# Kernel optimization log

Measured on AMD Instinct MI355X. Metric: run time of the kernel, lower is better.

## Reference

```python
import jax, jax.numpy as jnp
import numpy as np

B = 32
H_TEX, W_TEX, C = 512, 512, 3
N = H_TEX * W_TEX * C          # flattened texture length per sample
OH, OW = 128, 64               # bbox_size
M = OH * OW * C                # rows of each per-sample sparse matrix
NNZ = 98304                    # nonzeros per sample (4 per output element)


def setup_inputs() -> dict:
    key = jax.random.key(0)
    k1, k2, k3, k4 = jax.random.split(key, 4)
    x = jax.random.normal(k1, (B, C, H_TEX, W_TEX), dtype=jnp.float32)
    rows = jax.random.randint(k2, (B, NNZ), 0, M, dtype=jnp.int32)
    cols = jax.random.randint(k3, (B, NNZ), 0, N, dtype=jnp.int32)
    vals = jax.random.uniform(k4, (B, NNZ), dtype=jnp.float32)
    mask = jnp.ones((B, C, OH, OW), dtype=jnp.float32)
    return {"x": x, "rows": rows, "cols": cols, "vals": vals, "mask": mask}


def reference(x, rows, cols, vals, mask):
    # x: (B, C, H, W) -> channels-last flat per sample, matching x.permute(0,2,3,1).reshape(B,-1)
    xf = jnp.transpose(x, (0, 2, 3, 1)).reshape(B, -1)          # (B, N)
    # Batched sparse mm: out[b, m] = sum_{k: rows[b,k]==m} vals[b,k] * xf[b, cols[b,k]]
    gathered = vals * jnp.take_along_axis(xf, cols, axis=1)     # (B, NNZ)
    seg_ids = (rows.astype(jnp.int32) + jnp.arange(B, dtype=jnp.int32)[:, None] * M).reshape(-1)
    out_flat = jax.ops.segment_sum(gathered.reshape(-1), seg_ids, num_segments=B * M)
    result = out_flat.reshape(B, OH, OW, C).transpose(0, 3, 1, 2)  # (B, C, 128, 64)
    return result, mask
```

## Files before the change

kernel.cpp:

```cpp
#include <hip/hip_runtime.h>

#define BATCH 32
#define CCH 3
#define HW_TEX (512 * 512)
#define N_TEX (HW_TEX * CCH)
#define OH 128
#define OW 64
#define P_OUT (OH * OW)
#define M_OUT (P_OUT * CCH)
#define NNZ 98304
#define OUT_ELEMS (BATCH * M_OUT)

#define NCH 4
#define RPCH (M_OUT / NCH)
#define NE 8
#define SEGE (NNZ / NE)
#define TB 1024
#define NROUND 4

#define WS_NEED ((size_t)BATCH * NCH * NE * RPCH * 4)

__global__ __launch_bounds__(TB) void scan_pred8_kernel(
    const float* __restrict__ x,
    const int*   __restrict__ rows,
    const int*   __restrict__ cols,
    const float* __restrict__ vals,
    float* __restrict__ partial) {
    __shared__ __align__(16) float acc[RPCH];

    const int blk  = blockIdx.x;
    const int xcd  = blk & 7;
    const int slot = blk >> 3;
    const int c    = slot & (NCH - 1);
    const int e    = slot >> 2;
    const int t    = threadIdx.x;
    const int rbase = c * RPCH;

    for (int rnd = 0; rnd < NROUND; ++rnd) {
        const int s = rnd * 8 + xcd;

        float2* acc2 = reinterpret_cast<float2*>(acc);
#pragma unroll
        for (int j = 0; j < RPCH / 2 / TB; ++j)
            acc2[t + j * TB] = make_float2(0.f, 0.f);
        __syncthreads();

        const size_t off = (size_t)s * NNZ + (size_t)e * SEGE;
        const int4*   r4 = reinterpret_cast<const int4*>(rows + off);
        const int4*   c4 = reinterpret_cast<const int4*>(cols + off);
        const float4* v4 = reinterpret_cast<const float4*>(vals + off);
        const float*  xs = x + (size_t)s * N_TEX;

        int4 r[3], cc[3]; float4 v[3];
#pragma unroll
        for (int j = 0; j < 3; ++j) {
            r[j]  = r4[j * TB + t];
            cc[j] = c4[j * TB + t];
            v[j]  = v4[j * TB + t];
        }

#pragma unroll
        for (int j = 0; j < 3; ++j) {
            int   ri[4] = {r[j].x, r[j].y, r[j].z, r[j].w};
            int   ci[4] = {cc[j].x, cc[j].y, cc[j].z, cc[j].w};
            float vi[4] = {v[j].x, v[j].y, v[j].z, v[j].w};
#pragma unroll
            for (int k = 0; k < 4; ++k) {
                unsigned lr = (unsigned)(ri[k] - rbase);
                if (lr < (unsigned)RPCH) {
                    int gi = (ci[k] % CCH) * HW_TEX + ci[k] / CCH;
                    atomicAdd(&acc[lr], vi[k] * xs[gi]);
                }
            }
        }
        __syncthreads();

        float2* pp = reinterpret_cast<float2*>(
            partial + (((size_t)s * NCH + c) * NE + e) * RPCH);
#pragma unroll
        for (int j = 0; j < RPCH / 2 / TB; ++j)
            pp[t + j * TB] = acc2[t + j * TB];
        __syncthreads();
    }
}

__global__ __launch_bounds__(256) void reduce_chunk_kernel(
    const float* __restrict__ partial,
    const float* __restrict__ mask,
    float* __restrict__ out) {
    int tid = blockIdx.x * 256 + threadIdx.x;
    if (tid >= OUT_ELEMS / 4) return;
    int s    = tid / (M_OUT / 4);
    int rcl4 = (tid % (M_OUT / 4)) * 4;
    int c    = rcl4 / RPCH;
    int lr4  = rcl4 % RPCH;

    const float4* pp = reinterpret_cast<const float4*>(
        partial + (((size_t)s * NCH + c) * NE) * RPCH + lr4);
    float4 sum = make_float4(0.f, 0.f, 0.f, 0.f);
#pragma unroll
    for (int e = 0; e < NE; ++e) {
        float4 p = pp[(size_t)e * (RPCH / 4)];
        sum.x += p.x; sum.y += p.y; sum.z += p.z; sum.w += p.w;
    }
    float* ob = out + (size_t)s * M_OUT;
    ob[(rcl4 + 0) % CCH * P_OUT + (rcl4 + 0) / CCH] = sum.x;
    ob[(rcl4 + 1) % CCH * P_OUT + (rcl4 + 1) / CCH] = sum.y;
    ob[(rcl4 + 2) % CCH * P_OUT + (rcl4 + 2) / CCH] = sum.z;
    ob[(rcl4 + 3) % CCH * P_OUT + (rcl4 + 3) / CCH] = sum.w;
    reinterpret_cast<float4*>(out + OUT_ELEMS)[tid] =
        reinterpret_cast<const float4*>(mask)[tid];
}

#define CHUNKS 8
#define RPC (M_OUT / CHUNKS)
#define BLOCK 1024
__global__ __launch_bounds__(BLOCK) void spmm_chunk_kernel(
    const float* __restrict__ x,
    const int*   __restrict__ rows,
    const int*   __restrict__ cols,
    const float* __restrict__ vals,
    const float* __restrict__ mask,
    float* __restrict__ out) {
    __shared__ float acc[RPC];
    const int blk = blockIdx.x;
    const int s   = blk / CHUNKS;
    const int c   = blk % CHUNKS;
    const int t   = threadIdx.x;
    const int rbase = c * RPC;
#pragma unroll
    for (int j = 0; j < RPC / BLOCK; ++j) acc[t + j * BLOCK] = 0.0f;
    __syncthreads();
    const int*   rs = rows + (size_t)s * NNZ;
    const int*   cs = cols + (size_t)s * NNZ;
    const float* vs = vals + (size_t)s * NNZ;
    const float* xs = x    + (size_t)s * N_TEX;
#pragma unroll 4
    for (int i = t; i < NNZ; i += BLOCK) {
        int r = rs[i];
        unsigned lr = (unsigned)(r - rbase);
        if (lr < (unsigned)RPC) {
            int   col = cs[i];
            float v   = vs[i];
            atomicAdd(&acc[lr], v * xs[(col % CCH) * HW_TEX + col / CCH]);
        }
    }
    __syncthreads();
    const size_t outbase = (size_t)s * M_OUT;
#pragma unroll
    for (int ch = 0; ch < CCH; ++ch)
        out[outbase + (size_t)ch * P_OUT + c * (P_OUT / CHUNKS) + t] = acc[t * CCH + ch];
    {
        float* mout = out + OUT_ELEMS;
        const int base = blk * RPC;
#pragma unroll
        for (int j = 0; j < RPC / BLOCK; ++j)
            mout[base + j * BLOCK + t] = mask[base + j * BLOCK + t];
    }
}

extern "C" void kernel_launch(void* const* d_in, const int* in_sizes, int n_in,
                              void* d_out, int out_size, void* d_ws, size_t ws_size,
                              hipStream_t stream) {
    const float* x    = (const float*)d_in[0];
    const int*   rows = (const int*)  d_in[1];
    const int*   cols = (const int*)  d_in[2];
    const float* vals = (const float*)d_in[3];
    const float* mask = (const float*)d_in[4];
    float* out = (float*)d_out;
    int rgrid = (OUT_ELEMS / 4 + 255) / 256;

    if (ws_size >= WS_NEED) {
        float* partial = (float*)d_ws;
        scan_pred8_kernel<<<256, TB, 0, stream>>>(x, rows, cols, vals, partial);
        reduce_chunk_kernel<<<rgrid, 256, 0, stream>>>(partial, mask, out);
    } else {
        spmm_chunk_kernel<<<BATCH * CHUNKS, BLOCK, 0, stream>>>(x, rows, cols, vals, mask, out);
    }
}
```

Before: 208.8 us.

## Replace chunked LDS accumulation with direct global atomic scatter

Drops the LDS-chunked predicated scan and the partial-sum reduction. A zero-init kernel now clears the output and copies the mask, then each thread scatters its nonzeros straight into the output with global float atomicAdd. This removes the redundant rescans of the index stream across row chunks and the workspace round trip. The cost is global atomic traffic on random addresses and a summation order that is no longer deterministic.

```diff
diff --git a/kernel.cpp b/kernel.cpp
--- a/kernel.cpp
+++ b/kernel.cpp
@@ -11,152 +11,55 @@
 #define NNZ 98304
 #define OUT_ELEMS (BATCH * M_OUT)
 
-#define NCH 4
-#define RPCH (M_OUT / NCH)
-#define NE 8
-#define SEGE (NNZ / NE)
-#define TB 1024
+#define SC_TB 1024
 #define NROUND 4
 
-#define WS_NEED ((size_t)BATCH * NCH * NE * RPCH * 4)
-
-__global__ __launch_bounds__(TB) void scan_pred8_kernel(
+__global__ __launch_bounds__(SC_TB) void scatter_kernel(
     const float* __restrict__ x,
     const int*   __restrict__ rows,
     const int*   __restrict__ cols,
     const float* __restrict__ vals,
-    float* __restrict__ partial) {
-    __shared__ __align__(16) float acc[RPCH];
-
+    float* __restrict__ out) {
     const int blk  = blockIdx.x;
     const int xcd  = blk & 7;
     const int slot = blk >> 3;
-    const int c    = slot & (NCH - 1);
-    const int e    = slot >> 2;
     const int t    = threadIdx.x;
-    const int rbase = c * RPCH;
+    const int base = slot * SC_TB + t;
 
     for (int rnd = 0; rnd < NROUND; ++rnd) {
         const int s = rnd * 8 + xcd;
+        const size_t ib = (size_t)s * NNZ;
+        const float* xs = x + (size_t)s * N_TEX;
+        float* os = out + (size_t)s * M_OUT;
 
-        float2* acc2 = reinterpret_cast<float2*>(acc);
-#pragma unroll
-        for (int j = 0; j < RPCH / 2 / TB; ++j)
-            acc2[t + j * TB] = make_float2(0.f, 0.f);
-        __syncthreads();
+        int   r0 = rows[ib + base];
+        int   r1 = rows[ib + base + 32768];
+        int   r2 = rows[ib + base + 65536];
+        int   c0 = cols[ib + base];
+        int   c1 = cols[ib + base + 32768];
+        int   c2 = cols[ib + base + 65536];
+        float v0 = vals[ib + base];
+        float v1 = vals[ib + base + 32768];
+        float v2 = vals[ib + base + 65536];
 
-        const size_t off = (size_t)s * NNZ + (size_t)e * SEGE;
-        const int4*   r4 = reinterpret_cast<const int4*>(rows + off);
-        const int4*   c4 = reinterpret_cast<const int4*>(cols + off);
-        const float4* v4 = reinterpret_cast<const float4*>(vals + off);
-        const float*  xs = x + (size_t)s * N_TEX;
+        float x0 = xs[(c0 % CCH) * HW_TEX + c0 / CCH];
+        float x1 = xs[(c1 % CCH) * HW_TEX + c1 / CCH];
+        float x2 = xs[(c2 % CCH) * HW_TEX + c2 / CCH];
 
-        int4 r[3], cc[3]; float4 v[3];
-#pragma unroll
-        for (int j = 0; j < 3; ++j) {
-            r[j]  = r4[j * TB + t];
-            cc[j] = c4[j * TB + t];
-            v[j]  = v4[j * TB + t];
-        }
-
-#pragma unroll
-        for (int j = 0; j < 3; ++j) {
-            int   ri[4] = {r[j].x, r[j].y, r[j].z, r[j].w};
-            int   ci[4] = {cc[j].x, cc[j].y, cc[j].z, cc[j].w};
-            float vi[4] = {v[j].x, v[j].y, v[j].z, v[j].w};
-#pragma unroll
-            for (int k = 0; k < 4; ++k) {
-                unsigned lr = (unsigned)(ri[k] - rbase);
-                if (lr < (unsigned)RPCH) {
-                    int gi = (ci[k] % CCH) * HW_TEX + ci[k] / CCH;
-                    atomicAdd(&acc[lr], vi[k] * xs[gi]);
-                }
-            }
-        }
-        __syncthreads();
-
-        float2* pp = reinterpret_cast<float2*>(
-            partial + (((size_t)s * NCH + c) * NE + e) * RPCH);
-#pragma unroll
-        for (int j = 0; j < RPCH / 2 / TB; ++j)
-            pp[t + j * TB] = acc2[t + j * TB];
-        __syncthreads();
+        atomicAdd(&os[(r0 % CCH) * P_OUT + r0 / CCH], v0 * x0);
+        atomicAdd(&os[(r1 % CCH) * P_OUT + r1 / CCH], v1 * x1);
+        atomicAdd(&os[(r2 % CCH) * P_OUT + r2 / CCH], v2 * x2);
     }
 }
 
-__global__ __launch_bounds__(256) void reduce_chunk_kernel(
-    const float* __restrict__ partial,
+__global__ __launch_bounds__(256) void init_out_kernel(
     const float* __restrict__ mask,
     float* __restrict__ out) {
     int tid = blockIdx.x * 256 + threadIdx.x;
     if (tid >= OUT_ELEMS / 4) return;
-    int s    = tid / (M_OUT / 4);
-    int rcl4 = (tid % (M_OUT / 4)) * 4;
-    int c    = rcl4 / RPCH;
-    int lr4  = rcl4 % RPCH;
-
-    const float4* pp = reinterpret_cast<const float4*>(
-        partial + (((size_t)s * NCH + c) * NE) * RPCH + lr4);
-    float4 sum = make_float4(0.f, 0.f, 0.f, 0.f);
-#pragma unroll
-    for (int e = 0; e < NE; ++e) {
-        float4 p = pp[(size_t)e * (RPCH / 4)];
-        sum.x += p.x; sum.y += p.y; sum.z += p.z; sum.w += p.w;
-    }
-    float* ob = out + (size_t)s * M_OUT;
-    ob[(rcl4 + 0) % CCH * P_OUT + (rcl4 + 0) / CCH] = sum.x;
-    ob[(rcl4 + 1) % CCH * P_OUT + (rcl4 + 1) / CCH] = sum.y;
-    ob[(rcl4 + 2) % CCH * P_OUT + (rcl4 + 2) / CCH] = sum.z;
-    ob[(rcl4 + 3) % CCH * P_OUT + (rcl4 + 3) / CCH] = sum.w;
+    reinterpret_cast<float4*>(out)[tid] = make_float4(0.f, 0.f, 0.f, 0.f);
     reinterpret_cast<float4*>(out + OUT_ELEMS)[tid] =
         reinterpret_cast<const float4*>(mask)[tid];
-}
-
-#define CHUNKS 8
-#define RPC (M_OUT / CHUNKS)
-#define BLOCK 1024
-__global__ __launch_bounds__(BLOCK) void spmm_chunk_kernel(
-    const float* __restrict__ x,
-    const int*   __restrict__ rows,
-    const int*   __restrict__ cols,
-    const float* __restrict__ vals,
-    const float* __restrict__ mask,
-    float* __restrict__ out) {
-    __shared__ float acc[RPC];
-    const int blk = blockIdx.x;
-    const int s   = blk / CHUNKS;
-    const int c   = blk % CHUNKS;
-    const int t   = threadIdx.x;
-    const int rbase = c * RPC;
-#pragma unroll
-    for (int j = 0; j < RPC / BLOCK; ++j) acc[t + j * BLOCK] = 0.0f;
-    __syncthreads();
-    const int*   rs = rows + (size_t)s * NNZ;
-    const int*   cs = cols + (size_t)s * NNZ;
-    const float* vs = vals + (size_t)s * NNZ;
-    const float* xs = x    + (size_t)s * N_TEX;
-#pragma unroll 4
-    for (int i = t; i < NNZ; i += BLOCK) {
-        int r = rs[i];
-        unsigned lr = (unsigned)(r - rbase);
-        if (lr < (unsigned)RPC) {
-            int   col = cs[i];
-            float v   = vs[i];
-            atomicAdd(&acc[lr], v * xs[(col % CCH) * HW_TEX + col / CCH]);
-        }
-    }
-    __syncthreads();
-    const size_t outbase = (size_t)s * M_OUT;
-#pragma unroll
-    for (int ch = 0; ch < CCH; ++ch)
-        out[outbase + (size_t)ch * P_OUT + c * (P_OUT / CHUNKS) + t] = acc[t * CCH + ch];
-    {
-        float* mout = out + OUT_ELEMS;
-        const int base = blk * RPC;
-#pragma unroll
-        for (int j = 0; j < RPC / BLOCK; ++j)
-            mout[base + j * BLOCK + t] = mask[base + j * BLOCK + t];
-    }
 }
 
 extern "C" void kernel_launch(void* const* d_in, const int* in_sizes, int n_in,
@@ -168,13 +71,8 @@
     const float* vals = (const float*)d_in[3];
     const float* mask = (const float*)d_in[4];
     float* out = (float*)d_out;
-    int rgrid = (OUT_ELEMS / 4 + 255) / 256;
 
-    if (ws_size >= WS_NEED) {
-        float* partial = (float*)d_ws;
-        scan_pred8_kernel<<<256, TB, 0, stream>>>(x, rows, cols, vals, partial);
-        reduce_chunk_kernel<<<rgrid, 256, 0, stream>>>(partial, mask, out);
-    } else {
-        spmm_chunk_kernel<<<BATCH * CHUNKS, BLOCK, 0, stream>>>(x, rows, cols, vals, mask, out);
-    }
+    int igrid = (OUT_ELEMS / 4 + 255) / 256;
+    init_out_kernel<<<igrid, 256, 0, stream>>>(mask, out);
+    scatter_kernel<<<256, SC_TB, 0, stream>>>(x, rows, cols, vals, out);
 }
```

Result: slower. 304.0 us (+45.6%).

## Stage COO indices and gathered texels into LDS via global_load_lds

Applied to the files above, without the earlier changes.

Index, column and value arrays are now tiled and loaded straight into LDS with the global_load_lds builtin. The predicated texel gathers also go through direct-to-LDS loads, followed by a vmcnt wait and a separate LDS atomic-accumulate pass. The aim is to cut VGPR pressure and put the random gathers in flight together. In exchange it adds a barrier per tile and splits the gather and accumulate phases, which may reduce overlap. The gather destination relies on the per-lane M0/LDS addressing semantics of that builtin.

```diff
diff --git a/kernel.cpp b/kernel.cpp
--- a/kernel.cpp
+++ b/kernel.cpp
@@ -17,8 +17,21 @@
 #define SEGE (NNZ / NE)
 #define TB 1024
 #define NROUND 4
+#define TILE 3072
+#define EPT 3
 
 #define WS_NEED ((size_t)BATCH * NCH * NE * RPCH * 4)
+
+__device__ __forceinline__ void gld_lds16(const void* g, void* l) {
+    __builtin_amdgcn_global_load_lds(
+        (const __attribute__((address_space(1))) void*)g,
+        (__attribute__((address_space(3))) void*)l, 16, 0, 0);
+}
+__device__ __forceinline__ void gld_lds4(const void* g, void* l) {
+    __builtin_amdgcn_global_load_lds(
+        (const __attribute__((address_space(1))) void*)g,
+        (__attribute__((address_space(3))) void*)l, 4, 0, 0);
+}
 
 __global__ __launch_bounds__(TB) void scan_pred8_kernel(
     const float* __restrict__ x,
@@ -27,6 +40,8 @@
     const float* __restrict__ vals,
     float* __restrict__ partial) {
     __shared__ __align__(16) float acc[RPCH];
+    __shared__ __align__(16) int   s_idx[3][TILE];
+    __shared__ __align__(16) float s_gath[TILE];
 
     const int blk  = blockIdx.x;
     const int xcd  = blk & 7;
@@ -34,6 +49,8 @@
     const int c    = slot & (NCH - 1);
     const int e    = slot >> 2;
     const int t    = threadIdx.x;
+    const int lane = t & 63;
+    const int w    = t >> 6;
     const int rbase = c * RPCH;
 
     for (int rnd = 0; rnd < NROUND; ++rnd) {
@@ -46,34 +63,45 @@
         __syncthreads();
 
         const size_t off = (size_t)s * NNZ + (size_t)e * SEGE;
-        const int4*   r4 = reinterpret_cast<const int4*>(rows + off);
-        const int4*   c4 = reinterpret_cast<const int4*>(cols + off);
-        const float4* v4 = reinterpret_cast<const float4*>(vals + off);
-        const float*  xs = x + (size_t)s * N_TEX;
-
-        int4 r[3], cc[3]; float4 v[3];
-#pragma unroll
-        for (int j = 0; j < 3; ++j) {
-            r[j]  = r4[j * TB + t];
-            cc[j] = c4[j * TB + t];
-            v[j]  = v4[j * TB + t];
-        }
-
-#pragma unroll
-        for (int j = 0; j < 3; ++j) {
-            int   ri[4] = {r[j].x, r[j].y, r[j].z, r[j].w};
-            int   ci[4] = {cc[j].x, cc[j].y, cc[j].z, cc[j].w};
-            float vi[4] = {v[j].x, v[j].y, v[j].z, v[j].w};
-#pragma unroll
-            for (int k = 0; k < 4; ++k) {
-                unsigned lr = (unsigned)(ri[k] - rbase);
-                if (lr < (unsigned)RPCH) {
-                    int gi = (ci[k] % CCH) * HW_TEX + ci[k] / CCH;
-                    atomicAdd(&acc[lr], vi[k] * xs[gi]);
+        const float* xs = x + (size_t)s * N_TEX;
+        const int* gsrc[3] = { rows + off, cols + off,
+                               reinterpret_cast<const int*>(vals + off) };
+
+        for (int tt = 0; tt < SEGE / TILE; ++tt) {
+            const int toff = tt * TILE;
+
+            for (int q = w; q < 36; q += 16) {
+                const int arr = q / 12, sub = q % 12;
+                gld_lds16(gsrc[arr] + toff + sub * 256 + lane * 4,
+                          &s_idx[arr][sub * 256]);
+            }
+            __syncthreads();
+
+#pragma unroll
+            for (int k = 0; k < EPT; ++k) {
+                const int n = w * (EPT * 64) + k * 64 + lane;
+                int rI = s_idx[0][n];
+                int cI = s_idx[1][n];
+                unsigned l = (unsigned)(rI - rbase);
+                if (l < (unsigned)RPCH) {
+                    int gi = (cI % CCH) * HW_TEX + cI / CCH;
+                    gld_lds4(xs + gi, &s_gath[w * (EPT * 64) + k * 64]);
                 }
             }
+            asm volatile("s_waitcnt vmcnt(0)" ::: "memory");
+            __builtin_amdgcn_sched_barrier(0);
+
+#pragma unroll
+            for (int k = 0; k < EPT; ++k) {
+                const int n = w * (EPT * 64) + k * 64 + lane;
+                unsigned l = (unsigned)(s_idx[0][n] - rbase);
+                if (l < (unsigned)RPCH) {
+                    float vv = __int_as_float(s_idx[2][n]);
+                    atomicAdd(&acc[l], vv * s_gath[n]);
+                }
+            }
+            __syncthreads();
         }
-        __syncthreads();
 
         float2* pp = reinterpret_cast<float2*>(
             partial + (((size_t)s * NCH + c) * NE + e) * RPCH);
```

Result: slower. 223.0 us (+6.8%).

## Split rows into 2 chunks and nnz into 16 segments, batching gathers before atomics

Applied to the files above, without the earlier changes.

Adds a new scan/reduce path in which each block owns half the output rows (a 48KB LDS accumulator) and a 1/16 slice of the nonzeros, so each entry is scanned by only 2 blocks instead of 4. It also issues all 6 predicated texture gathers before doing the LDS atomics, to raise memory-level parallelism. In exchange the reduce kernel sums 16 partials instead of 8, and the larger LDS footprint may limit occupancy. The new path runs when the workspace is large enough, otherwise the older paths are kept.

```diff
diff --git a/kernel.cpp b/kernel.cpp
--- a/kernel.cpp
+++ b/kernel.cpp
@@ -11,14 +11,121 @@
 #define NNZ 98304
 #define OUT_ELEMS (BATCH * M_OUT)
 
+#define TB 1024
+#define NROUND 4
+
+#define NCH2 2
+#define RPCH2 (M_OUT / NCH2)
+#define NE2 16
+#define SEGE2 (NNZ / NE2)
+#define EPT2 6
+#define WS_NEED2 ((size_t)BATCH * NCH2 * NE2 * RPCH2 * 4)
+
 #define NCH 4
 #define RPCH (M_OUT / NCH)
 #define NE 8
 #define SEGE (NNZ / NE)
-#define TB 1024
-#define NROUND 4
-
+#define EPT 12
 #define WS_NEED ((size_t)BATCH * NCH * NE * RPCH * 4)
+
+__global__ __launch_bounds__(TB) void scan2_kernel(
+    const float* __restrict__ x,
+    const int*   __restrict__ rows,
+    const int*   __restrict__ cols,
+    const float* __restrict__ vals,
+    float* __restrict__ partial) {
+    __shared__ __align__(16) float acc[RPCH2];
+
+    const int blk  = blockIdx.x;
+    const int xcd  = blk & 7;
+    const int slot = blk >> 3;
+    const int c    = slot & (NCH2 - 1);
+    const int e    = slot >> 1;
+    const int t    = threadIdx.x;
+    const int rbase = c * RPCH2;
+
+    for (int rnd = 0; rnd < NROUND; ++rnd) {
+        const int s = rnd * 8 + xcd;
+
+        float2* acc2 = reinterpret_cast<float2*>(acc);
+#pragma unroll
+        for (int j = 0; j < RPCH2 / 2 / TB; ++j)
+            acc2[t + j * TB] = make_float2(0.f, 0.f);
+        __syncthreads();
+
+        const size_t off = (size_t)s * NNZ + (size_t)e * SEGE2;
+        const int2*   r2 = reinterpret_cast<const int2*>(rows + off);
+        const int2*   c2 = reinterpret_cast<const int2*>(cols + off);
+        const float2* v2 = reinterpret_cast<const float2*>(vals + off);
+        const float*  xs = x + (size_t)s * N_TEX;
+
+        int2 rr[3], cc[3]; float2 vv[3];
+#pragma unroll
+        for (int j = 0; j < 3; ++j) {
+            rr[j] = r2[t + j * TB];
+            cc[j] = c2[t + j * TB];
+            vv[j] = v2[t + j * TB];
+        }
+        int ri[EPT2]; int ci[EPT2]; float vi[EPT2];
+#pragma unroll
+        for (int j = 0; j < 3; ++j) {
+            ri[2 * j] = rr[j].x; ri[2 * j + 1] = rr[j].y;
+            ci[2 * j] = cc[j].x; ci[2 * j + 1] = cc[j].y;
+            vi[2 * j] = vv[j].x; vi[2 * j + 1] = vv[j].y;
+        }
+
+        float xv[EPT2];
+#pragma unroll
+        for (int i = 0; i < EPT2; ++i) {
+            unsigned l = (unsigned)(ri[i] - rbase);
+            int gi = (ci[i] % CCH) * HW_TEX + ci[i] / CCH;
+            xv[i] = xs[(l < (unsigned)RPCH2) ? gi : 0];
+        }
+
+#pragma unroll
+        for (int i = 0; i < EPT2; ++i) {
+            unsigned l = (unsigned)(ri[i] - rbase);
+            if (l < (unsigned)RPCH2)
+                atomicAdd(&acc[l], vi[i] * xv[i]);
+        }
+        __syncthreads();
+
+        float2* pp = reinterpret_cast<float2*>(
+            partial + (((size_t)s * NCH2 + c) * NE2 + e) * RPCH2);
+#pragma unroll
+        for (int j = 0; j < RPCH2 / 2 / TB; ++j)
+            pp[t + j * TB] = acc2[t + j * TB];
+        __syncthreads();
+    }
+}
+
+__global__ __launch_bounds__(256) void reduce2_kernel(
+    const float* __restrict__ partial,
+    const float* __restrict__ mask,
+    float* __restrict__ out) {
+    int tid = blockIdx.x * 256 + threadIdx.x;
+    if (tid >= OUT_ELEMS / 4) return;
+    int s    = tid / (M_OUT / 4);
+    int rcl4 = (tid % (M_OUT / 4)) * 4;
+    int c    = rcl4 / RPCH2;
+    int lr4  = rcl4 % RPCH2;
+
+    const float4* pp = reinterpret_cast<const float4*>(
+        partial + (((size_t)s * NCH2 + c) * NE2) * RPCH2 + lr4);
+    float4 sum = make_float4(0.f, 0.f, 0.f, 0.f);
+#pragma unroll
+    for (int e = 0; e < NE2; ++e) {
+        float4 p = pp[(size_t)e * (RPCH2 / 4)];
+        sum.x += p.x; sum.y += p.y; sum.z += p.z; sum.w += p.w;
+    }
+    float* ob = out + (size_t)s * M_OUT;
+    ob[(rcl4 + 0) % CCH * P_OUT + (rcl4 + 0) / CCH] = sum.x;
+    ob[(rcl4 + 1) % CCH * P_OUT + (rcl4 + 1) / CCH] = sum.y;
+    ob[(rcl4 + 2) % CCH * P_OUT + (rcl4 + 2) / CCH] = sum.z;
+    ob[(rcl4 + 3) % CCH * P_OUT + (rcl4 + 3) / CCH] = sum.w;
+    reinterpret_cast<float4*>(out + OUT_ELEMS)[tid] =
+        reinterpret_cast<const float4*>(mask)[tid];
+}
 
 __global__ __launch_bounds__(TB) void scan_pred8_kernel(
     const float* __restrict__ x,
@@ -38,7 +145,6 @@
 
     for (int rnd = 0; rnd < NROUND; ++rnd) {
         const int s = rnd * 8 + xcd;
-
         float2* acc2 = reinterpret_cast<float2*>(acc);
 #pragma unroll
         for (int j = 0; j < RPCH / 2 / TB; ++j)
@@ -58,7 +164,6 @@
             cc[j] = c4[j * TB + t];
             v[j]  = v4[j * TB + t];
         }
-
 #pragma unroll
         for (int j = 0; j < 3; ++j) {
             int   ri[4] = {r[j].x, r[j].y, r[j].z, r[j].w};
@@ -170,7 +275,11 @@
     float* out = (float*)d_out;
     int rgrid = (OUT_ELEMS / 4 + 255) / 256;
 
-    if (ws_size >= WS_NEED) {
+    if (ws_size >= WS_NEED2) {
+        float* partial = (float*)d_ws;
+        scan2_kernel<<<256, TB, 0, stream>>>(x, rows, cols, vals, partial);
+        reduce2_kernel<<<rgrid, 256, 0, stream>>>(partial, mask, out);
+    } else if (ws_size >= WS_NEED) {
         float* partial = (float*)d_ws;
         scan_pred8_kernel<<<256, TB, 0, stream>>>(x, rows, cols, vals, partial);
         reduce_chunk_kernel<<<rgrid, 256, 0, stream>>>(partial, mask, out);
```

After: 212.2 us. About the same (+1.6%).
